# Kernel optimization log

Hardware: AMD Instinct MI355X
Metric: run time of the kernel (lower is better)

The kernel has to match this reference:

```python
import jax, jax.numpy as jnp
import numpy as np

B, T, N, K, C = 4, 12, 2000, 8, 32
AGG_N = 4  # mean, max, min, std
EPS = 1e-5


def sparsify(a, k):
    # keep top-k entries per row, zero the rest (torch.topk + torch.where)
    thr = jax.lax.top_k(a, k)[0][..., -1:]
    return jnp.where(a < thr, jnp.zeros_like(a), a)


def aggregate(I, adj):
    # I: (b,t,n,f), adj: (b,n,n) row-sparsified with K nonzeros per row
    deg = jnp.sum(adj, axis=-1)[:, None, :, None]              # (b,1,n,1)
    mean = jnp.einsum('bnm,btmf->btnf', adj, I) / deg
    meansq = jnp.einsum('bnm,btmf->btnf', adj, I * I) / deg
    std = jnp.sqrt(jax.nn.relu(meansq - mean * mean) + EPS)
    vals, idx = jax.lax.top_k(adj, K)                          # (b,n,K)
    nb = jax.vmap(lambda Ib, ib: Ib[:, ib])(I, idx)            # (b,t,n,K,f)
    valid = (vals > 0)[:, None, :, :, None]
    mx = jnp.max(jnp.where(valid, nb, -jnp.inf), axis=3)
    mn = jnp.min(jnp.where(valid, nb, jnp.inf), axis=3)
    return jnp.concatenate([mean, mx, mn, std], axis=3)


def stower(x, adj, Theta, bias, masking, use_scalers):
    # x: (b,c,t,n) -> out: (b,o,t,n)
    I = jnp.transpose(x, (0, 2, 3, 1))                          # (b,t,n,c)
    m = aggregate(I, adj)
    if masking:
        m = jnp.where(jnp.isnan(m), 6.0, m)
        m = jnp.where(jnp.isinf(m), 0.0, m)
        m = jnp.minimum(m, 6.0)
    if use_scalers:
        deg = jnp.sum((adj > 0).astype(m.dtype), axis=-1)       # (b,n)
        s = jnp.log1p(deg)[:, None, :, None]
        m = jnp.concatenate([m, m * s, m / s], axis=3)
    out = jnp.einsum('btji,io->btjo', m, Theta) + bias
    return jnp.transpose(out, (0, 3, 1, 2))


def tcn(x, W, b):
    # tcn_layer2 with act='linear': tanh(conv1x1(x) + x)
    return jnp.tanh(jnp.einsum('oc,bctn->botn', W, x) + b[None, :, None, None] + x)


def setup_inputs():
    key = jax.random.key(0)
    ks = jax.random.split(key, 14)
    stdv = 1.0 / np.sqrt(C)
    u = lambda k, shape: jax.random.uniform(k, shape, jnp.float32, -stdv, stdv)
    return {
        'X': jax.random.normal(ks[0], (B, T, N, 1), jnp.float32),
        'adj': jax.random.uniform(ks[1], (N, N), jnp.float32),
        'adj_mask': jax.random.uniform(ks[2], (N, N), jnp.float32),
        'Theta0': u(ks[3], (AGG_N * 1, C)),   # len(agg)*len(['identity'])*in_variables
        'bias0': u(ks[4], (C,)),
        'Wt0': u(ks[5], (C, C)),
        'bt0': u(ks[6], (C,)),
        'Theta1': u(ks[7], (AGG_N * 3 * C, C)),  # len(agg)*len(scalers)*channels
        'bias1': u(ks[8], (C,)),
        'Wt1': u(ks[9], (C, C)),
        'bt1': u(ks[10], (C,)),
        'Wout': u(ks[11], (1, C)),
        'bout': u(ks[12], (1,)),
        'batch_seen': 0,
        'epoch': 0,
        'train': 0,
    }


def reference(X, adj, adj_mask, Theta0, bias0, Wt0, bt0, Theta1, bias1, Wt1, bt1, Wout, bout, batch_seen, epoch, train):
    x0 = X[:, None, :, :, 0]                                   # (b,1,t,n)
    adj_s = sparsify(jnp.broadcast_to(adj, (B, N, N)), K)
    adjm_s = sparsify(jnp.broadcast_to(adj_mask, (B, N, N)), K)
    h = stower(x0, adjm_s, Theta0, bias0, True, False)         # s_layer0 (masking, identity scaler)
    h = tcn(h, Wt0, bt0)                                       # t_layer0
    h = jax.nn.relu(stower(h, adj_s, Theta1, bias1, False, True))
    h = jax.nn.relu(tcn(h, Wt1, bt1))
    y = jnp.einsum('oc,bctn->botn', Wout, h) + bout[None, :, None, None]
    return y.reshape(B, T, N)
```

## Files before the change

### kernel.cpp

```cpp
#include <hip/hip_runtime.h>
#include <hip/hip_bf16.h>
#include <math.h>

#define BB 4
#define TT 12
#define NN 2000
#define KK 8
#define CC 32
#define EPSF 1e-5f
#define LISTCAP 16
#define NSITES (BB * TT * NN)

typedef unsigned short u16;
typedef __bf16 bf16x8 __attribute__((ext_vector_type(8)));
typedef float  f32x4  __attribute__((ext_vector_type(4)));

__device__ __forceinline__ u16 f2bf(float x) {
    union { __hip_bfloat16 h; u16 u; } c;
    c.h = __float2bfloat16(x);
    return c.u;
}
__device__ __forceinline__ float bf2f(u16 u) {
    return __uint_as_float(((unsigned)u) << 16);
}
__device__ __forceinline__ float mask6(float v) {
    if (isnan(v)) v = 6.0f;
    if (isinf(v)) v = 0.0f;
    return fminf(v, 6.0f);
}

__global__ __launch_bounds__(256)
void topk_prep(const float* __restrict__ adj, const float* __restrict__ adjm,
               int* __restrict__ t_idx, float* __restrict__ t_val,
               int* __restrict__ t_cnt, float* __restrict__ t_deg,
               float* __restrict__ t_ideg, float2* __restrict__ t_sc)
{
    __shared__ float sTop[4][8];
    __shared__ float sDeg[4];
    __shared__ int   sCp[4];
    __shared__ int   sStrictIdx[8];
    __shared__ float sStrictVal[8];
    __shared__ int   sTieIdx[16];
    __shared__ int   nStrict, nTie;
    __shared__ float sThr;

    const int tid  = threadIdx.x;
    const int lane = tid & 63;
    const int wid  = tid >> 6;

    const int grow = blockIdx.x;
    const int mat = (grow >= NN) ? 1 : 0;
    const int row = grow - mat * NN;
    const float* src = (mat == 0 ? adjm : adj) + (size_t)row * NN;
    const float4* src4 = (const float4*)src;

    if (tid == 0) { nStrict = 0; nTie = 0; }

    const float4 v0 = src4[tid];
    const float4 v1 = (tid < 244) ? src4[256 + tid]
                                  : make_float4(-1.f, -1.f, -1.f, -1.f);
    const float vv[8] = {v0.x, v0.y, v0.z, v0.w, v1.x, v1.y, v1.z, v1.w};

    float a[8];
    #pragma unroll
    for (int j = 0; j < 8; ++j) a[j] = vv[j];
    #define CE(i, j) { float _mx = fmaxf(a[i], a[j]); float _mn = fminf(a[i], a[j]); a[i] = _mx; a[j] = _mn; }
    CE(0,1) CE(2,3) CE(4,5) CE(6,7)
    CE(0,2) CE(1,3) CE(4,6) CE(5,7)
    CE(1,2) CE(5,6)
    CE(0,4) CE(1,5) CE(2,6) CE(3,7)
    CE(2,4) CE(3,5)
    CE(1,2) CE(3,4) CE(5,6)
    #undef CE

    float key[8];
    #pragma unroll
    for (int j = 0; j < 8; ++j) key[j] = a[j];
    #pragma unroll
    for (int d = 1; d < 64; d <<= 1) {
        float ok[8], c[8];
        #pragma unroll
        for (int j = 0; j < 8; ++j) ok[j] = __shfl_xor(key[j], d, 64);
        #pragma unroll
        for (int j = 0; j < 8; ++j) c[j] = fmaxf(key[j], ok[7 - j]);
        #pragma unroll
        for (int st = 4; st >= 1; st >>= 1) {
            #pragma unroll
            for (int j = 0; j < 8; ++j) {
                if ((j & st) == 0 && (j | st) < 8) {
                    float hi = fmaxf(c[j], c[j | st]);
                    float lo = fminf(c[j], c[j | st]);
                    c[j] = hi; c[j | st] = lo;
                }
            }
        }
        #pragma unroll
        for (int j = 0; j < 8; ++j) key[j] = c[j];
    }
    if (lane == 0) {
        #pragma unroll
        for (int j = 0; j < 8; ++j) sTop[wid][j] = key[j];
    }
    __syncthreads();

    if (tid == 0) {
        int p0 = 0, p1 = 0, p2 = 0, p3 = 0;
        float t = -1.f;
        for (int r = 0; r < 8; ++r) {
            const float c0 = (p0 < 8) ? sTop[0][p0] : -2.f;
            const float c1 = (p1 < 8) ? sTop[1][p1] : -2.f;
            const float c2 = (p2 < 8) ? sTop[2][p2] : -2.f;
            const float c3 = (p3 < 8) ? sTop[3][p3] : -2.f;
            float bv = c0; int best = 0;
            if (c1 > bv) { bv = c1; best = 1; }
            if (c2 > bv) { bv = c2; best = 2; }
            if (c3 > bv) { bv = c3; best = 3; }
            if (best == 0) ++p0; else if (best == 1) ++p1;
            else if (best == 2) ++p2; else ++p3;
            t = bv;
        }
        sThr = t;
    }
    __syncthreads();
    const float thr = sThr;

    float degp = 0.f; int cp = 0;
    #pragma unroll
    for (int s = 0; s < 8; ++s) {
        const float v = vv[s];
        const int e = (s < 4) ? (tid * 4 + s) : ((256 + tid) * 4 + (s - 4));
        const bool ge = (v >= thr);
        degp += ge ? v : 0.f;
        cp   += (ge && v > 0.f) ? 1 : 0;
        if (v > thr) {
            int p = atomicAdd(&nStrict, 1);
            if (p < 8) { sStrictIdx[p] = e; sStrictVal[p] = v; }
        } else if (v == thr) {
            int p = atomicAdd(&nTie, 1);
            if (p < 16) sTieIdx[p] = e;
        }
    }
    #pragma unroll
    for (int off = 32; off >= 1; off >>= 1) {
        degp += __shfl_xor(degp, off, 64);
        cp   += __shfl_xor(cp, off, 64);
    }
    if (lane == 0) { sDeg[wid] = degp; sCp[wid] = cp; }
    __syncthreads();

    if (tid == 0) {
        const float deg = sDeg[0] + sDeg[1] + sDeg[2] + sDeg[3];
        const int cnt_pos = sCp[0] + sCp[1] + sCp[2] + sCp[3];
        int m = nStrict; if (m > 8) m = 8;
        int nt = nTie;   if (nt > 16) nt = 16;
        for (int i = 1; i < nt; ++i) {
            int v = sTieIdx[i]; int j = i - 1;
            while (j >= 0 && sTieIdx[j] > v) { sTieIdx[j + 1] = sTieIdx[j]; --j; }
            sTieIdx[j + 1] = v;
        }
        const size_t ob = (size_t)grow * LISTCAP;
        for (int j = 0; j < m; ++j) {
            t_idx[ob + j] = sStrictIdx[j];
            t_val[ob + j] = sStrictVal[j];
        }
        const int need = 8 - m;
        for (int j = 0; j < need; ++j) {
            t_idx[ob + m + j] = sTieIdx[j];
            t_val[ob + m + j] = thr;
        }
        int extra = nt - need;
        if (extra > 8) extra = 8; if (extra < 0) extra = 0;
        for (int j = 0; j < extra; ++j) {
            t_idx[ob + 8 + j] = sTieIdx[need + j];
            t_val[ob + 8 + j] = thr;
        }
        t_cnt[grow]  = 8 + extra;
        t_deg[grow]  = deg;
        t_ideg[grow] = 1.0f / deg;
        const float s1 = log1pf((float)cnt_pos);
        t_sc[grow]   = make_float2(s1, 1.0f / s1);
    }
}

__global__ __launch_bounds__(256)
void stower0_tcn0(const float* __restrict__ X,
                  const int* __restrict__ t_idx, const float* __restrict__ t_val,
                  const int* __restrict__ t_cnt, const float* __restrict__ t_deg,
                  const float* __restrict__ Theta0, const float* __restrict__ bias0,
                  const float* __restrict__ Wt0, const float* __restrict__ bt0,
                  const float* __restrict__ Theta1, const float* __restrict__ Wt1,
                  u16* __restrict__ thHi, u16* __restrict__ thLo,
                  u16* __restrict__ wtHi, u16* __restrict__ wtLo,
                  float* __restrict__ I1)
{
    const int tid = threadIdx.x;
    if (blockIdx.x >= NSITES / 256) {
        const int pb = blockIdx.x - NSITES / 256;
        if (pb < 12) {
            const int base = pb * 1024;
            #pragma unroll
            for (int t = 0; t < 4; ++t) {
                const int i = base + t * 256 + tid;
                const int r = i >> 5, o = i & 31;
                const int jm = r >> 7, k = r & 127;
                const int tile = jm * 2 + (o >> 4), n = o & 15;
                const float v = Theta1[i];
                const u16 hi = f2bf(v);
                const int idx = (tile * 16 + n) * 128 + (((k >> 3) ^ n) << 3) + (k & 7);
                thHi[idx] = hi;
                thLo[idx] = f2bf(v - bf2f(hi));
            }
        } else {
            #pragma unroll
            for (int t = 0; t < 4; ++t) {
                const int i = t * 256 + tid;
                const float v = Wt1[i];
                const u16 hi = f2bf(v);
                wtHi[i] = hi;
                wtLo[i] = f2bf(v - bf2f(hi));
            }
        }
        return;
    }

    const int site = blockIdx.x * 256 + tid;
    const int n  = site % NN;
    const int bt = site / NN;
    const float* xrow = X + (size_t)bt * NN;

    const size_t base = (size_t)n * LISTCAP;
    const int cnt   = t_cnt[n];
    const float deg = t_deg[n];
    float wsum = 0.f, wsq = 0.f, mx = -INFINITY, mn = INFINITY;
    for (int j = 0; j < cnt; ++j) {
        int   id = t_idx[base + j];
        float w  = t_val[base + j];
        float xv = xrow[id];
        wsum = fmaf(w, xv, wsum);
        wsq  = fmaf(w * xv, xv, wsq);
        if (j < KK && w > 0.f) { mx = fmaxf(mx, xv); mn = fminf(mn, xv); }
    }
    float mean = wsum / deg;
    float var  = wsq / deg - mean * mean;
    float sd   = sqrtf(fmaxf(var, 0.f) + EPSF);
    float m0 = mask6(mean), m1 = mask6(mx), m2 = mask6(mn), m3 = mask6(sd);

    float h0[CC];
    #pragma unroll
    for (int c = 0; c < CC; ++c) {
        float v = bias0[c];
        v = fmaf(m0, Theta0[0 * CC + c], v);
        v = fmaf(m1, Theta0[1 * CC + c], v);
        v = fmaf(m2, Theta0[2 * CC + c], v);
        v = fmaf(m3, Theta0[3 * CC + c], v);
        h0[c] = v;
    }
    float* op = I1 + (size_t)site * CC;
    #pragma unroll
    for (int c = 0; c < CC; ++c) {
        float acc = bt0[c] + h0[c];
        #pragma unroll
        for (int k = 0; k < CC; ++k) acc = fmaf(Wt0[c * CC + k], h0[k], acc);
        op[c] = tanhf(acc);
    }
}

__global__ __launch_bounds__(256, 3)
void stower1_fused(const float* __restrict__ I1,
                   const int* __restrict__ t_idx, const float* __restrict__ t_val,
                   const int* __restrict__ t_cnt, const float* __restrict__ t_ideg,
                   const u16* __restrict__ thHi, const u16* __restrict__ thLo,
                   const u16* __restrict__ wtHi, const u16* __restrict__ wtLo,
                   const float2* __restrict__ t_sc,
                   const float* __restrict__ bias1, const float* __restrict__ bt1,
                   const float* __restrict__ Wout, const float* __restrict__ bout,
                   float* __restrict__ out)
{
    __shared__ u16 sBlo[96 * 128];
    __shared__ alignas(16) u16 uSpace[12288];
    __shared__ float sPart[64];

    u16*   mT  = uSpace;
    u16*   hHi = uSpace;
    u16*   hLo = hHi + 32 * 40;
    float* h32 = (float*)((char*)uSpace + 5120);

    const int tid  = threadIdx.x;
    const int lane = tid & 63;
    const int w    = tid >> 6;
    const int m15  = lane & 15;
    const int q    = lane >> 4;
    const int hf   = w & 1;
    const int st   = w >> 1;
    const int ot   = w >> 1;
    const int st2  = w & 1;

    const int ag = tid >> 5;
    const int af = tid & 31;
    const int afh = af >> 3, afl = af & 7;

    for (int i = tid; i < 1536; i += 256)
        ((float4*)uSpace)[i] = ((const float4*)thHi)[i];
    __syncthreads();
    bf16x8 bH[3][4];
    #pragma unroll
    for (int j3 = 0; j3 < 3; ++j3) {
        const int tile = 2 * j3 + hf;
        #pragma unroll
        for (int ks = 0; ks < 4; ++ks)
            bH[j3][ks] = *(const bf16x8*)&uSpace[(tile * 16 + m15) * 128 +
                                                 (((ks * 4 + q) ^ m15) << 3)];
    }
    __syncthreads();
    for (int i = tid; i < 1536; i += 256)
        ((float4*)sBlo)[i] = ((const float4*)thLo)[i];
    const bf16x8 bwh = *(const bf16x8*)&wtHi[(ot * 16 + m15) * 32 + q * 8];
    const bf16x8 bwl = *(const bf16x8*)&wtLo[(ot * 16 + m15) * 32 + q * 8];
    const float b1o   = bias1[hf * 16 + m15];
    const float bt1o  = bt1[ot * 16 + m15];
    const float wouto = Wout[ot * 16 + m15];
    const float boutv = bout[0];

    #pragma unroll 1
    for (int mb = 0; mb < 3; ++mb) {
        const int sbase = (blockIdx.x * 3 + mb) * 32;

        #pragma unroll 1
        for (int r = 0; r < 4; ++r) {
            const int sl2  = ag * 4 + r;
            const int site = sbase + sl2;
            const int n    = site % NN;
            const int bt   = site / NN;
            const size_t rbase = (size_t)(NN + n) * LISTCAP;
            const int cnt    = t_cnt[NN + n];
            const float ideg = t_ideg[NN + n];
            const float* Ibt = I1 + (size_t)bt * NN * CC;

            const int4   i0 = *(const int4*)&t_idx[rbase];
            const int4   i1 = *(const int4*)&t_idx[rbase + 4];
            const float4 w0 = *(const float4*)&t_val[rbase];
            const float4 w1 = *(const float4*)&t_val[rbase + 4];

            const float x0 = Ibt[(size_t)i0.x * CC + af];
            const float x1 = Ibt[(size_t)i0.y * CC + af];
            const float x2 = Ibt[(size_t)i0.z * CC + af];
            const float x3 = Ibt[(size_t)i0.w * CC + af];
            const float x4 = Ibt[(size_t)i1.x * CC + af];
            const float x5 = Ibt[(size_t)i1.y * CC + af];
            const float x6 = Ibt[(size_t)i1.z * CC + af];
            const float x7 = Ibt[(size_t)i1.w * CC + af];

            float wsum = 0.f, wsq = 0.f, mx = -INFINITY, mn = INFINITY;
            #define AGG(wv, xv) do { \
                wsum = fmaf(wv, xv, wsum); wsq = fmaf(wv * xv, xv, wsq); \
                mx = fmaxf(mx, xv); mn = fminf(mn, xv); } while (0)
            AGG(w0.x, x0); AGG(w0.y, x1); AGG(w0.z, x2); AGG(w0.w, x3);
            AGG(w1.x, x4); AGG(w1.y, x5); AGG(w1.z, x6); AGG(w1.w, x7);
            #undef AGG
            if (cnt > 8) {
                for (int j = 8; j < cnt; ++j) {
                    int   id = t_idx[rbase + j];
                    float wv = t_val[rbase + j];
                    float xv = Ibt[(size_t)id * CC + af];
                    wsum = fmaf(wv, xv, wsum);
                    wsq  = fmaf(wv * xv, xv, wsq);
                }
            }
            const float mean = wsum * ideg;
            const float var  = wsq * ideg - mean * mean;
            const float sd   = sqrtf(fmaxf(var, 0.f) + EPSF);

            const int sx = sl2 & 15;
            const int b  = sl2 * 128;
            const int ia  = b + (((0  + afh) ^ sx) << 3) + afl;
            const int ib  = b + (((4  + afh) ^ sx) << 3) + afl;
            const int ic  = b + (((8  + afh) ^ sx) << 3) + afl;
            const int id_ = b + (((12 + afh) ^ sx) << 3) + afl;
            u16 h0 = f2bf(mean); mT[ia]  = h0; mT[4096 + ia]  = f2bf(mean - bf2f(h0));
            u16 h1 = f2bf(mx);   mT[ib]  = h1; mT[4096 + ib]  = f2bf(mx   - bf2f(h1));
            u16 h2 = f2bf(mn);   mT[ic]  = h2; mT[4096 + ic]  = f2bf(mn   - bf2f(h2));
            u16 h3 = f2bf(sd);   mT[id_] = h3; mT[4096 + id_] = f2bf(sd   - bf2f(h3));
        }
        __syncthreads();

        f32x4 acc[3];
        #pragma unroll
        for (int j3 = 0; j3 < 3; ++j3) acc[j3] = (f32x4){0.f, 0.f, 0.f, 0.f};
        const int arow = (st * 16 + m15) * 128;
        #pragma unroll
        for (int ks = 0; ks < 4; ++ks) {
            const int koff = (((ks * 4 + q) ^ m15) << 3);
            const bf16x8 aH = *(const bf16x8*)&mT[arow + koff];
            const bf16x8 aL = *(const bf16x8*)&mT[4096 + arow + koff];
            #pragma unroll
            for (int j3 = 0; j3 < 3; ++j3) {
                const bf16x8 bL = *(const bf16x8*)&sBlo[((2 * j3 + hf) * 16 + m15) * 128 + koff];
                acc[j3] = __builtin_amdgcn_mfma_f32_16x16x32_bf16(aH, bH[j3][ks], acc[j3], 0, 0, 0);
                acc[j3] = __builtin_amdgcn_mfma_f32_16x16x32_bf16(aH, bL,          acc[j3], 0, 0, 0);
                acc[j3] = __builtin_amdgcn_mfma_f32_16x16x32_bf16(aL, bH[j3][ks], acc[j3], 0, 0, 0);
            }
        }
        __syncthreads();

        #pragma unroll
        for (int r = 0; r < 4; ++r) {
            const int sl2  = st * 16 + q * 4 + r;
            const int site = sbase + sl2;
            const int n    = site % NN;
            const float2 sc = t_sc[NN + n];
            float h = acc[0][r] + sc.x * acc[1][r] + sc.y * acc[2][r] + b1o;
            h = fmaxf(h, 0.f);
            const int o = hf * 16 + m15;
            const u16 hi = f2bf(h);
            hHi[sl2 * 40 + o] = hi;
            hLo[sl2 * 40 + o] = f2bf(h - bf2f(hi));
            h32[sl2 * 33 + o] = h;
        }
        __syncthreads();

        f32x4 c2 = (f32x4){0.f, 0.f, 0.f, 0.f};
        {
            const bf16x8 ahh = *(const bf16x8*)&hHi[(st2 * 16 + m15) * 40 + q * 8];
            const bf16x8 ahl = *(const bf16x8*)&hLo[(st2 * 16 + m15) * 40 + q * 8];
            c2 = __builtin_amdgcn_mfma_f32_16x16x32_bf16(ahh, bwh, c2, 0, 0, 0);
            c2 = __builtin_amdgcn_mfma_f32_16x16x32_bf16(ahh, bwl, c2, 0, 0, 0);
            c2 = __builtin_amdgcn_mfma_f32_16x16x32_bf16(ahl, bwh, c2, 0, 0, 0);
        }
        float p[4];
        #pragma unroll
        for (int r = 0; r < 4; ++r) {
            const int sl2 = st2 * 16 + q * 4 + r;
            const float hres = h32[sl2 * 33 + ot * 16 + m15];
            float yv = tanhf(c2[r] + bt1o + hres);
            yv = fmaxf(yv, 0.f);
            p[r] = yv * wouto;
            #pragma unroll
            for (int mk = 1; mk <= 8; mk <<= 1)
                p[r] += __shfl_xor(p[r], mk, 64);
        }
        float selv  = (m15 & 1) ? p[1] : p[0];
        float selv2 = (m15 & 1) ? p[3] : p[2];
        selv = (m15 & 2) ? selv2 : selv;
        if (m15 < 4) sPart[ot * 32 + st2 * 16 + q * 4 + m15] = selv;
        __syncthreads();

        if (tid < 32) out[sbase + tid] = sPart[tid] + sPart[32 + tid] + boutv;
    }
}

extern "C" void kernel_launch(void* const* d_in, const int* in_sizes, int n_in,
                              void* d_out, int out_size, void* d_ws, size_t ws_size,
                              hipStream_t stream)
{
    const float* X      = (const float*)d_in[0];
    const float* adj    = (const float*)d_in[1];
    const float* adjm   = (const float*)d_in[2];
    const float* Theta0 = (const float*)d_in[3];
    const float* bias0  = (const float*)d_in[4];
    const float* Wt0    = (const float*)d_in[5];
    const float* bt0    = (const float*)d_in[6];
    const float* Theta1 = (const float*)d_in[7];
    const float* bias1  = (const float*)d_in[8];
    const float* Wt1    = (const float*)d_in[9];
    const float* bt1    = (const float*)d_in[10];
    const float* Wout   = (const float*)d_in[11];
    const float* bout   = (const float*)d_in[12];
    (void)in_sizes; (void)n_in; (void)out_size; (void)ws_size;

    char* p = (char*)d_ws;
    int*    t_idx  = (int*)p;    p += (size_t)2 * NN * LISTCAP * sizeof(int);
    float*  t_val  = (float*)p;  p += (size_t)2 * NN * LISTCAP * sizeof(float);
    int*    t_cnt  = (int*)p;    p += (size_t)2 * NN * sizeof(int);
    float*  t_deg  = (float*)p;  p += (size_t)2 * NN * sizeof(float);
    float*  t_ideg = (float*)p;  p += (size_t)2 * NN * sizeof(float);
    float2* t_sc   = (float2*)p; p += (size_t)2 * NN * sizeof(float2);
    float*  I1     = (float*)p;  p += (size_t)NSITES * CC * sizeof(float);
    u16*    thHi   = (u16*)p;    p += (size_t)96 * 128 * sizeof(u16);
    u16*    thLo   = (u16*)p;    p += (size_t)96 * 128 * sizeof(u16);
    u16*    wtHi   = (u16*)p;    p += (size_t)1024 * sizeof(u16);
    u16*    wtLo   = (u16*)p;    p += (size_t)1024 * sizeof(u16);

    hipLaunchKernelGGL(topk_prep, dim3(2 * NN), dim3(256), 0, stream,
                       adj, adjm, t_idx, t_val, t_cnt, t_deg, t_ideg, t_sc);
    hipLaunchKernelGGL(stower0_tcn0, dim3(NSITES / 256 + 13), dim3(256), 0, stream,
                       X, t_idx, t_val, t_cnt, t_deg, Theta0, bias0, Wt0, bt0,
                       Theta1, Wt1, thHi, thLo, wtHi, wtLo, I1);
    hipLaunchKernelGGL(stower1_fused, dim3(NSITES / 96), dim3(256), 0, stream,
                       I1, t_idx, t_val, t_cnt, t_ideg,
                       thHi, thLo, wtHi, wtLo, t_sc,
                       bias1, bt1, Wout, bout, (float*)d_out);
}
```

Baseline: 179.7 us.

## Shrink stower1 LDS footprint to raise occupancy to four blocks per CU

Reduces shared memory in the fused second-layer kernel by loading the high Theta fragments straight from global memory into registers and keeping the third low-part tile in registers, so only two tiles stay in LDS. sPart is moved into the reused uSpace buffer, and a trailing barrier is added to guard that reuse. Launch bounds go from 3 to 4 blocks per CU, the gather loop is unrolled by 2, and 64-bit index math becomes 32-bit. The extra register-resident fragments may raise register pressure or cause spills under the tighter bound, and the added barrier costs a sync per iteration.

```diff
diff --git a/kernel.cpp b/kernel.cpp
--- a/kernel.cpp
+++ b/kernel.cpp
@@ -265,7 +265,7 @@
     }
 }
 
-__global__ __launch_bounds__(256, 3)
+__global__ __launch_bounds__(256, 4)
 void stower1_fused(const float* __restrict__ I1,
                    const int* __restrict__ t_idx, const float* __restrict__ t_val,
                    const int* __restrict__ t_cnt, const float* __restrict__ t_ideg,
@@ -276,14 +276,14 @@
                    const float* __restrict__ Wout, const float* __restrict__ bout,
                    float* __restrict__ out)
 {
-    __shared__ u16 sBlo[96 * 128];
-    __shared__ alignas(16) u16 uSpace[12288];
-    __shared__ float sPart[64];
+    __shared__ u16 sBlo[64 * 128];
+    __shared__ alignas(16) u16 uSpace[8192];
 
     u16*   mT  = uSpace;
     u16*   hHi = uSpace;
     u16*   hLo = hHi + 32 * 40;
-    float* h32 = (float*)((char*)uSpace + 5120);
+    float* h32   = (float*)((char*)uSpace + 5120);
+    float* sPart = (float*)((char*)uSpace + 9472);
 
     const int tid  = threadIdx.x;
     const int lane = tid & 63;
@@ -299,20 +299,21 @@
     const int af = tid & 31;
     const int afh = af >> 3, afl = af & 7;
 
-    for (int i = tid; i < 1536; i += 256)
-        ((float4*)uSpace)[i] = ((const float4*)thHi)[i];
-    __syncthreads();
     bf16x8 bH[3][4];
     #pragma unroll
     for (int j3 = 0; j3 < 3; ++j3) {
         const int tile = 2 * j3 + hf;
         #pragma unroll
         for (int ks = 0; ks < 4; ++ks)
-            bH[j3][ks] = *(const bf16x8*)&uSpace[(tile * 16 + m15) * 128 +
-                                                 (((ks * 4 + q) ^ m15) << 3)];
-    }
-    __syncthreads();
-    for (int i = tid; i < 1536; i += 256)
+            bH[j3][ks] = *(const bf16x8*)&thHi[(tile * 16 + m15) * 128 +
+                                               (((ks * 4 + q) ^ m15) << 3)];
+    }
+    bf16x8 bL2[4];
+    #pragma unroll
+    for (int ks = 0; ks < 4; ++ks)
+        bL2[ks] = *(const bf16x8*)&thLo[((4 + hf) * 16 + m15) * 128 +
+                                        (((ks * 4 + q) ^ m15) << 3)];
+    for (int i = tid; i < 1024; i += 256)
         ((float4*)sBlo)[i] = ((const float4*)thLo)[i];
     const bf16x8 bwh = *(const bf16x8*)&wtHi[(ot * 16 + m15) * 32 + q * 8];
     const bf16x8 bwl = *(const bf16x8*)&wtLo[(ot * 16 + m15) * 32 + q * 8];
@@ -325,7 +326,7 @@
     for (int mb = 0; mb < 3; ++mb) {
         const int sbase = (blockIdx.x * 3 + mb) * 32;
 
-        #pragma unroll 1
+        #pragma unroll 2
         for (int r = 0; r < 4; ++r) {
             const int sl2  = ag * 4 + r;
             const int site = sbase + sl2;
@@ -341,14 +342,14 @@
             const float4 w0 = *(const float4*)&t_val[rbase];
             const float4 w1 = *(const float4*)&t_val[rbase + 4];
 
-            const float x0 = Ibt[(size_t)i0.x * CC + af];
-            const float x1 = Ibt[(size_t)i0.y * CC + af];
-            const float x2 = Ibt[(size_t)i0.z * CC + af];
-            const float x3 = Ibt[(size_t)i0.w * CC + af];
-            const float x4 = Ibt[(size_t)i1.x * CC + af];
-            const float x5 = Ibt[(size_t)i1.y * CC + af];
-            const float x6 = Ibt[(size_t)i1.z * CC + af];
-            const float x7 = Ibt[(size_t)i1.w * CC + af];
+            const float x0 = Ibt[i0.x * CC + af];
+            const float x1 = Ibt[i0.y * CC + af];
+            const float x2 = Ibt[i0.z * CC + af];
+            const float x3 = Ibt[i0.w * CC + af];
+            const float x4 = Ibt[i1.x * CC + af];
+            const float x5 = Ibt[i1.y * CC + af];
+            const float x6 = Ibt[i1.z * CC + af];
+            const float x7 = Ibt[i1.w * CC + af];
 
             float wsum = 0.f, wsq = 0.f, mx = -INFINITY, mn = INFINITY;
             #define AGG(wv, xv) do { \
@@ -361,7 +362,7 @@
                 for (int j = 8; j < cnt; ++j) {
                     int   id = t_idx[rbase + j];
                     float wv = t_val[rbase + j];
-                    float xv = Ibt[(size_t)id * CC + af];
+                    float xv = Ibt[id * CC + af];
                     wsum = fmaf(wv, xv, wsum);
                     wsq  = fmaf(wv * xv, xv, wsq);
                 }
@@ -394,7 +395,9 @@
             const bf16x8 aL = *(const bf16x8*)&mT[4096 + arow + koff];
             #pragma unroll
             for (int j3 = 0; j3 < 3; ++j3) {
-                const bf16x8 bL = *(const bf16x8*)&sBlo[((2 * j3 + hf) * 16 + m15) * 128 + koff];
+                const bf16x8 bL = (j3 < 2)
+                    ? *(const bf16x8*)&sBlo[((2 * j3 + hf) * 16 + m15) * 128 + koff]
+                    : bL2[ks];
                 acc[j3] = __builtin_amdgcn_mfma_f32_16x16x32_bf16(aH, bH[j3][ks], acc[j3], 0, 0, 0);
                 acc[j3] = __builtin_amdgcn_mfma_f32_16x16x32_bf16(aH, bL,          acc[j3], 0, 0, 0);
                 acc[j3] = __builtin_amdgcn_mfma_f32_16x16x32_bf16(aL, bH[j3][ks], acc[j3], 0, 0, 0);
@@ -445,6 +448,7 @@
         __syncthreads();
 
         if (tid < 32) out[sbase + tid] = sPart[tid] + sPart[32 + tid] + boutv;
+        __syncthreads();
     }
 }
 
```

Measured after the change: 173.9 us (median of 3 runs). 3.2% less time.
